# Performance work log

Measured on AMD Instinct MI355X. Metric: run time of the kernel, lower is better.

The kernel has to match this reference:

```python
import jax, jax.numpy as jnp
import numpy as np

MIN_NEAR = 0.05
DENSITY_SCALE = 1.0
BOUND = 1.0  # spherical scene bounds radius
GEO = 15


def _density_mlp(x, dW1, db1, dW2, db2, dW3, db3):
    h = jax.nn.relu(x @ dW1 + db1)
    h = jax.nn.relu(h @ dW2 + db2)
    h = h @ dW3 + db3  # [M, 1+GEO]
    sigma = jnp.exp(jnp.clip(h[..., 0], -15.0, 15.0))  # trunc_exp
    return sigma, h[..., 1:]


def _color_mlp(d, geo, cW1, cb1, cW2, cb2, cW3, cb3):
    h = jnp.concatenate([d, geo], axis=-1)
    h = jax.nn.relu(h @ cW1 + cb1)
    h = jax.nn.relu(h @ cW2 + cb2)
    return jax.nn.sigmoid(h @ cW3 + cb3)


def _comp_weights(deltas, sigmas):
    # alpha compositing: w_i = alpha_i * prod_{j<i}(1 - alpha_j)
    alphas = 1.0 - jnp.exp(-deltas * sigmas)
    trans = jnp.cumprod(
        jnp.concatenate([jnp.ones_like(alphas[:, :1]), 1.0 - alphas + 1e-15], axis=-1),
        axis=-1)[:, :-1]
    return alphas * trans


def _sample_pdf(bins, weights, n_samples):
    # deterministic importance resampling (eval mode); bins [N,T-1], weights [N,T-2]
    weights = weights + 1e-5
    pdf = weights / jnp.sum(weights, axis=-1, keepdims=True)
    cdf = jnp.cumsum(pdf, axis=-1)
    cdf = jnp.concatenate([jnp.zeros_like(cdf[:, :1]), cdf], axis=-1)  # [N, T-1]
    u = jnp.linspace(0.5 / n_samples, 1.0 - 0.5 / n_samples, n_samples)
    u = jnp.broadcast_to(u, (bins.shape[0], n_samples))
    inds = jax.vmap(lambda c, uu: jnp.searchsorted(c, uu, side='right'))(cdf, u)
    below = jnp.clip(inds - 1, 0, cdf.shape[-1] - 1)
    above = jnp.clip(inds, 0, cdf.shape[-1] - 1)
    cdf_g0 = jnp.take_along_axis(cdf, below, axis=-1)
    cdf_g1 = jnp.take_along_axis(cdf, above, axis=-1)
    bmax = bins.shape[-1] - 1
    bins_g0 = jnp.take_along_axis(bins, jnp.clip(below, 0, bmax), axis=-1)
    bins_g1 = jnp.take_along_axis(bins, jnp.clip(above, 0, bmax), axis=-1)
    denom = jnp.where(cdf_g1 - cdf_g0 < 1e-5, 1.0, cdf_g1 - cdf_g0)
    t = (u - cdf_g0) / denom
    return bins_g0 + t * (bins_g1 - bins_g0)


def _run(rays_o, rays_d, dW1, db1, dW2, db2, dW3, db3,
         cW1, cb1, cW2, cb2, cW3, cb3, num_steps, upsample_steps):
    N = rays_o.shape[0]
    # get_z_val_bounds: ray/sphere intersection, sphere radius BOUND at origin
    b = jnp.sum(rays_o * rays_d, axis=-1)
    c = jnp.sum(rays_o * rays_o, axis=-1) - BOUND ** 2
    disc = jnp.maximum(b * b - c, 0.0)
    z_max = jnp.maximum(-b + jnp.sqrt(disc), MIN_NEAR + 1e-3)
    z_min = jnp.full_like(z_max, MIN_NEAR)
    # get_foreground_z_vals: per-ray linspace (perturb=False)
    t = jnp.linspace(0.0, 1.0, num_steps)
    z_vals = z_min[:, None] + (z_max - z_min)[:, None] * t[None, :]
    z_vals = jnp.clip(z_vals, z_min[:, None], z_max[:, None])
    xyzs = rays_o[:, None, :] + rays_d[:, None, :] * z_vals[..., None]
    sigma, geo = _density_mlp(xyzs.reshape(-1, 3), dW1, db1, dW2, db2, dW3, db3)
    sigma = sigma.reshape(N, num_steps)
    geo = geo.reshape(N, num_steps, GEO)

    # upsample_z_values: importance resampling from coarse weights
    deltas = z_vals[:, 1:] - z_vals[:, :-1]
    aug = jnp.concatenate([deltas, deltas[:, -1:]], axis=-1)
    w_coarse = _comp_weights(aug, DENSITY_SCALE * sigma)
    z_mid = 0.5 * (z_vals[:, :-1] + z_vals[:, 1:])
    new_z = jax.lax.stop_gradient(_sample_pdf(z_mid, w_coarse[:, 1:-1], upsample_steps))
    new_xyzs = rays_o[:, None, :] + rays_d[:, None, :] * new_z[..., None]
    new_sigma, new_geo = _density_mlp(new_xyzs.reshape(-1, 3), dW1, db1, dW2, db2, dW3, db3)
    new_sigma = new_sigma.reshape(N, upsample_steps)
    new_geo = new_geo.reshape(N, upsample_steps, GEO)

    # sort/gather merge of coarse + fine samples
    z_all = jnp.concatenate([z_vals, new_z], axis=1)
    order = jnp.argsort(z_all, axis=1)
    z_vals = jnp.take_along_axis(z_all, order, axis=1)  # [N, T]
    xyzs = jnp.take_along_axis(jnp.concatenate([xyzs, new_xyzs], axis=1), order[..., None], axis=1)
    sigma = jnp.take_along_axis(jnp.concatenate([sigma, new_sigma], axis=1), order, axis=1)
    geo = jnp.take_along_axis(jnp.concatenate([geo, new_geo], axis=1), order[..., None], axis=1)

    deltas = z_vals[:, 1:] - z_vals[:, :-1]
    aug = jnp.concatenate([deltas, deltas[:, -1:]], axis=-1)
    weights = _comp_weights(aug, DENSITY_SCALE * sigma)  # [N, T]

    mask = weights > 1e-4
    dirs = jnp.broadcast_to(rays_d[:, None, :], xyzs.shape).reshape(-1, 3)
    rgb = _color_mlp(dirs, geo.reshape(-1, GEO), cW1, cb1, cW2, cb2, cW3, cb3)
    rgbs = jnp.where(mask.reshape(-1, 1), rgb, 0.0).reshape(N, -1, 3)

    weights_sum = jnp.sum(weights, axis=-1)
    depth = jnp.sum(weights * z_vals, axis=-1)
    image = jnp.sum(weights[..., None] * rgbs, axis=-2)
    bg = 206.0 / 255.0
    image = image + (1.0 - weights_sum)[..., None] * bg

    # pairwise distortion loss (the (z_shifted - z_shifted) term in the source is identically zero)
    sample_dist = 1.0 / num_steps
    z_shift = jnp.concatenate([z_vals[:, 1:], jnp.full((N, 1), sample_dist, z_vals.dtype)], axis=-1)
    mid_zs = 0.5 * z_vals + 0.5 * z_shift
    pair = jnp.abs(mid_zs[:, None, :] - mid_zs[:, :, None]) * (weights[:, None, :] * weights[:, :, None])
    loss = jnp.sum(pair, axis=(1, 2)) / (depth + 1e-6)
    loss = jnp.where(loss < 1e-3, 0.0, loss)  # cutoff
    return jnp.concatenate([image, depth[:, None], loss[:, None]], axis=-1)  # [N, 5]


def setup_inputs() -> dict:
    key = jax.random.key(0)
    ks = jax.random.split(key, 16)
    N, H = 2048, 256
    rays_o = 0.1 * jax.random.normal(ks[0], (N, 3), jnp.float32)  # near scene centre
    rd = jax.random.normal(ks[1], (N, 3), jnp.float32)
    rays_d = rd / jnp.linalg.norm(rd, axis=-1, keepdims=True)

    def w(k, shape):
        return jax.random.normal(k, shape, jnp.float32) * (1.0 / np.sqrt(shape[0]))

    return {
        'rays_o': rays_o, 'rays_d': rays_d,
        'dW1': w(ks[2], (3, H)), 'db1': jnp.zeros(H, jnp.float32),
        'dW2': w(ks[3], (H, H)), 'db2': jnp.zeros(H, jnp.float32),
        'dW3': w(ks[4], (H, 1 + GEO)), 'db3': jnp.zeros(1 + GEO, jnp.float32),
        'cW1': w(ks[5], (3 + GEO, H)), 'cb1': jnp.zeros(H, jnp.float32),
        'cW2': w(ks[6], (H, H)), 'cb2': jnp.zeros(H, jnp.float32),
        'cW3': w(ks[7], (H, 3)), 'cb3': jnp.zeros(3, jnp.float32),
        'num_steps': 128, 'upsample_steps': 128,
    }


def reference(rays_o, rays_d, dW1, db1, dW2, db2, dW3, db3,
              cW1, cb1, cW2, cb2, cW3, cb3, num_steps, upsample_steps):
    return _run(rays_o, rays_d, dW1, db1, dW2, db2, dW3, db3,
                cW1, cb1, cW2, cb2, cW3, cb3, num_steps, upsample_steps)
```

## Files before the change

kernel.cpp:

```cpp
#include <hip/hip_runtime.h>


typedef float f32x4 __attribute__((ext_vector_type(4)));
typedef __bf16 bf16x8 __attribute__((ext_vector_type(8)));
typedef __bf16 bf16x4 __attribute__((ext_vector_type(4)));
typedef unsigned short u16x8 __attribute__((ext_vector_type(8)));
typedef unsigned short u16x4 __attribute__((ext_vector_type(4)));

#define NRAYS 2048
#define NSTEP 128
#define MIN_NEAR 0.05f

#define OFF_D1 0
#define OFF_D2 8192
#define OFF_D3 73728
#define OFF_C1 77824
#define OFF_C2 86016
#define OFF_C3 151552
#define PACK_TOTAL 155648

__device__ __forceinline__ unsigned short f2bf(float f) {
  __bf16 h = (__bf16)f;
  return __builtin_bit_cast(unsigned short, h);
}
__device__ __forceinline__ u16x4 pack4(float a, float b, float c, float d) {
  bf16x4 h;
  h[0] = (__bf16)a; h[1] = (__bf16)b; h[2] = (__bf16)c; h[3] = (__bf16)d;
  return __builtin_bit_cast(u16x4, h);
}

__device__ __forceinline__ float ray_z(const float* __restrict__ ro,
                                       const float* __restrict__ rd, int r, int i) {
  float ox = ro[r * 3], oy = ro[r * 3 + 1], oz = ro[r * 3 + 2];
  float dx = rd[r * 3], dy = rd[r * 3 + 1], dz = rd[r * 3 + 2];
  float b = ox * dx + oy * dy + oz * dz;
  float c = ox * ox + oy * oy + oz * oz - 1.0f;
  float disc = fmaxf(b * b - c, 0.0f);
  float zmax = fmaxf(-b + sqrtf(disc), MIN_NEAR + 1e-3f);
  float zmin = MIN_NEAR;
  float tt = (float)i / 127.0f;
  float zz = zmin + (zmax - zmin) * tt;
  return fminf(fmaxf(zz, zmin), zmax);
}

__device__ __forceinline__ float wave_iscan(float v, int lane) {
#pragma unroll
  for (int off = 1; off < 64; off <<= 1) {
    float y = __shfl_up(v, off, 64);
    if (lane >= off) v += y;
  }
  return v;
}
__device__ __forceinline__ float block_iscan(float v, float* part, int lane, int wid) {
  float s = wave_iscan(v, lane);
  if (lane == 63) part[wid] = s;
  __syncthreads();
  float pre = 0.f;
  if (wid > 0) pre += part[0];
  if (wid > 1) pre += part[1];
  if (wid > 2) pre += part[2];
  return s + pre;
}

__device__ __forceinline__ void pack_std(const float* __restrict__ W,
                                         unsigned short* __restrict__ dst,
                                         int idx, int K, int Norig, int NT) {
  int per = NT * 512;
  int kt = idx / per, rm = idx % per;
  int nt = rm >> 9, lane = (rm >> 3) & 63, j = rm & 7;
  int k = kt * 32 + ((lane >> 4) << 3) + j;
  int n = nt * 16 + (lane & 15);
  float v = (k < K && n < Norig) ? W[k * Norig + n] : 0.0f;
  dst[idx] = f2bf(v);
}

__global__ void k_pack_all(const float* __restrict__ dW1, const float* __restrict__ dW2,
                           const float* __restrict__ dW3, const float* __restrict__ cW1,
                           const float* __restrict__ cW2, const float* __restrict__ cW3,
                           unsigned short* __restrict__ Wp) {
  int idx = blockIdx.x * 256 + threadIdx.x;
  if (idx < OFF_D2) {
    pack_std(dW1, Wp + OFF_D1, idx - OFF_D1, 3, 256, 16);
  } else if (idx < OFF_D3) {
    pack_std(dW2, Wp + OFF_D2, idx - OFF_D2, 256, 256, 16);
  } else if (idx < OFF_C1) {
    int j2 = idx - OFF_D3;
    int lane = (j2 >> 3) & 63, jj = j2 & 7, kt = j2 >> 9;
    int k = kt * 32 + ((lane >> 4) << 3) + jj;
    int n = lane & 15;
    Wp[idx] = f2bf(dW3[k * 16 + ((n + 1) & 15)]);
  } else if (idx < OFF_C2) {
    int j2 = idx - OFF_C1;
    int nt = j2 >> 9, lane = (j2 >> 3) & 63, jj = j2 & 7;
    int k = ((lane >> 4) << 3) + jj;
    int n = nt * 16 + (lane & 15);
    float v = 0.0f;
    if (k < 15) v = cW1[(3 + k) * 256 + n];
    else if (k >= 16 && k < 19) v = cW1[(k - 16) * 256 + n];
    Wp[idx] = f2bf(v);
  } else if (idx < OFF_C3) {
    pack_std(cW2, Wp + OFF_C2, idx - OFF_C2, 256, 256, 16);
  } else if (idx < PACK_TOTAL) {
    pack_std(cW3, Wp + OFF_C3, idx - OFF_C3, 256, 3, 1);
  }
}


__device__ __forceinline__ void mlp_l1(const unsigned short* xb, unsigned short* buf,
                                       const bf16x8 (&w1r)[4], const float* sb1,
                                       int wid, int quad, int col) {
#pragma unroll
  for (int h = 0; h < 2; ++h) {
    f32x4 acc[8];
#pragma unroll
    for (int i = 0; i < 8; ++i) acc[i] = (f32x4){0.f, 0.f, 0.f, 0.f};
    int p0 = (h * 2) * 16 + col, p1 = (h * 2 + 1) * 16 + col;
    bf16x8 x0 = *reinterpret_cast<const bf16x8*>(&xb[p0 * 32 + ((quad ^ (p0 & 3)) * 8)]);
    bf16x8 x1 = *reinterpret_cast<const bf16x8*>(&xb[p1 * 32 + ((quad ^ (p1 & 3)) * 8)]);
#pragma unroll
    for (int ntl = 0; ntl < 4; ++ntl) {
      acc[ntl * 2 + 0] = __builtin_amdgcn_mfma_f32_16x16x32_bf16(w1r[ntl], x0, acc[ntl * 2 + 0], 0, 0, 0);
      acc[ntl * 2 + 1] = __builtin_amdgcn_mfma_f32_16x16x32_bf16(w1r[ntl], x1, acc[ntl * 2 + 1], 0, 0, 0);
    }
#pragma unroll
    for (int ntl = 0; ntl < 4; ++ntl) {
      int n = (wid * 4 + ntl) * 16 + quad * 4;
      f32x4 bv = *reinterpret_cast<const f32x4*>(&sb1[n]);
#pragma unroll
      for (int j = 0; j < 2; ++j) {
        int p = (h * 2 + j) * 16 + col;
        *reinterpret_cast<u16x4*>(&buf[p * 256 + (((n >> 3) ^ (p & 31)) * 8) + (n & 7)]) =
            pack4(fmaxf(acc[ntl * 2 + j][0] + bv[0], 0.f), fmaxf(acc[ntl * 2 + j][1] + bv[1], 0.f),
                  fmaxf(acc[ntl * 2 + j][2] + bv[2], 0.f), fmaxf(acc[ntl * 2 + j][3] + bv[3], 0.f));
      }
    }
  }
}

__device__ __forceinline__ void l2_half_compute(const unsigned short* buf,
                                                const bf16x8 (&w2r)[8][4],
                                                f32x4 (&acc)[8], int h, int quad, int col) {
#pragma unroll
  for (int i = 0; i < 8; ++i) acc[i] = (f32x4){0.f, 0.f, 0.f, 0.f};
#pragma unroll
  for (int kt = 0; kt < 8; ++kt) {
    int p0 = (h * 2) * 16 + col, p1 = (h * 2 + 1) * 16 + col;
    bf16x8 x0 = *reinterpret_cast<const bf16x8*>(&buf[p0 * 256 + (((kt * 4 + quad) ^ (p0 & 31)) * 8)]);
    bf16x8 x1 = *reinterpret_cast<const bf16x8*>(&buf[p1 * 256 + (((kt * 4 + quad) ^ (p1 & 31)) * 8)]);
#pragma unroll
    for (int ntl = 0; ntl < 4; ++ntl) {
      acc[ntl * 2 + 0] = __builtin_amdgcn_mfma_f32_16x16x32_bf16(w2r[kt][ntl], x0, acc[ntl * 2 + 0], 0, 0, 0);
      acc[ntl * 2 + 1] = __builtin_amdgcn_mfma_f32_16x16x32_bf16(w2r[kt][ntl], x1, acc[ntl * 2 + 1], 0, 0, 0);
    }
  }
}

__device__ __forceinline__ void l2_half_write(unsigned short* buf, const f32x4 (&acc)[8],
                                              const float* sb2, int h, int wid, int quad, int col) {
#pragma unroll
  for (int ntl = 0; ntl < 4; ++ntl) {
    int n = (wid * 4 + ntl) * 16 + quad * 4;
    f32x4 bv = *reinterpret_cast<const f32x4*>(&sb2[n]);
#pragma unroll
    for (int j = 0; j < 2; ++j) {
      int p = (h * 2 + j) * 16 + col;
      *reinterpret_cast<u16x4*>(&buf[p * 256 + (((n >> 3) ^ (p & 31)) * 8) + (n & 7)]) =
          pack4(fmaxf(acc[ntl * 2 + j][0] + bv[0], 0.f), fmaxf(acc[ntl * 2 + j][1] + bv[1], 0.f),
                fmaxf(acc[ntl * 2 + j][2] + bv[2], 0.f), fmaxf(acc[ntl * 2 + j][3] + bv[3], 0.f));
    }
  }
}

template <bool FIRST>
__global__ __launch_bounds__(256, 2)
void k_density(const float* __restrict__ ro, const float* __restrict__ rd,
               const float* __restrict__ zin,
               const unsigned short* __restrict__ Wp1, const float* __restrict__ b1,
               const unsigned short* __restrict__ Wp2, const float* __restrict__ b2,
               const unsigned short* __restrict__ Wp3, const float* __restrict__ b3,
               unsigned short* __restrict__ gout, float* __restrict__ sig,
               float* __restrict__ z_f) {
  __shared__ __align__(16) unsigned short buf[64 * 256];
  __shared__ __align__(16) unsigned short xb[64 * 32];
  __shared__ __align__(16) unsigned short sW3[4096];
  __shared__ __align__(16) float sb1[256];
  __shared__ __align__(16) float sb2[256];
  __shared__ __align__(16) float sb3[16];
  __shared__ __align__(16) float ssig[256];
  __shared__ __align__(16) float sred[16];
  const int t = threadIdx.x;
  const int lane = t & 63, wid = t >> 6, quad = lane >> 4, col = lane & 15;
  const int p_ = t >> 2, g_ = t & 3;

  sb1[t] = b1[t];
  sb2[t] = b2[t];
  if (t < 16) sb3[t] = b3[(t + 1) & 15];
  { const u16x8* s = (const u16x8*)Wp3; u16x8* d = (u16x8*)sW3;
    d[t] = s[t]; d[t + 256] = s[t + 256]; }

  bf16x8 w1r[4], w2r[8][4];
#pragma unroll
  for (int ntl = 0; ntl < 4; ++ntl)
    w1r[ntl] = *reinterpret_cast<const bf16x8*>(Wp1 + ((wid * 4 + ntl) * 64 + lane) * 8);
#pragma unroll
  for (int kt = 0; kt < 8; ++kt)
#pragma unroll
    for (int ntl = 0; ntl < 4; ++ntl)
      w2r[kt][ntl] = *reinterpret_cast<const bf16x8*>(Wp2 + ((kt * 16 + wid * 4 + ntl) * 64 + lane) * 8);

#pragma unroll 1
  for (int tt = 0; tt < 4; ++tt) {
    const int P0 = blockIdx.x * 256 + tt * 64;
    {
      u16x8 pk = {0, 0, 0, 0, 0, 0, 0, 0};
      if (g_ == 0) {
        int P = P0 + p_;
        int rr_ = P >> 7, ii = P & 127;
        float zz;
        if constexpr (FIRST) zz = ray_z(ro, rd, rr_, ii);
        else zz = zin[P];
        pk[0] = f2bf(ro[rr_ * 3 + 0] + rd[rr_ * 3 + 0] * zz);
        pk[1] = f2bf(ro[rr_ * 3 + 1] + rd[rr_ * 3 + 1] * zz);
        pk[2] = f2bf(ro[rr_ * 3 + 2] + rd[rr_ * 3 + 2] * zz);
      }
      *reinterpret_cast<u16x8*>(&xb[p_ * 32 + ((g_ ^ (p_ & 3)) * 8)]) = pk;
    }
    __syncthreads();
    mlp_l1(xb, buf, w1r, sb1, wid, quad, col);
    __syncthreads();
    f32x4 acc[8];
    l2_half_compute(buf, w2r, acc, 0, quad, col);
    __syncthreads();
    l2_half_write(buf, acc, sb2, 0, wid, quad, col);
    l2_half_compute(buf, w2r, acc, 1, quad, col);
    __syncthreads();
    l2_half_write(buf, acc, sb2, 1, wid, quad, col);
    __syncthreads();
    {
      const int p = wid * 16 + col;
      f32x4 a3 = {0.f, 0.f, 0.f, 0.f};
#pragma unroll
      for (int kt = 0; kt < 8; ++kt) {
        bf16x8 w = *reinterpret_cast<const bf16x8*>(&sW3[(kt * 64 + lane) * 8]);
        bf16x8 xx = *reinterpret_cast<const bf16x8*>(&buf[p * 256 + (((kt * 4 + quad) ^ (p & 31)) * 8)]);
        a3 = __builtin_amdgcn_mfma_f32_16x16x32_bf16(w, xx, a3, 0, 0, 0);
      }
      int n0 = quad * 4;
      float v0 = a3[0] + sb3[n0], v1 = a3[1] + sb3[n0 + 1];
      float v2 = a3[2] + sb3[n0 + 2], v3 = a3[3] + sb3[n0 + 3];
      if (quad == 3) {
        float sgm = __expf(fminf(fmaxf(v3, -15.f), 15.f));
        sig[P0 + p] = sgm;
        if constexpr (FIRST) ssig[tt * 64 + p] = sgm;
        v3 = 0.0f;
      }
      *reinterpret_cast<u16x4*>(gout + (size_t)(P0 + p) * 16 + n0) = pack4(v0, v1, v2, v3);
    }
  }

  if constexpr (FIRST) {
    __syncthreads();
    float* psz = reinterpret_cast<float*>(buf);
    float* pmid = psz + 256;
    float* pcdf = psz + 512;
    float* psw = psz + 768;
    const int segw = t >> 7;
    const int i = t & 127;
    const int seg = segw * 128;
    const int rg = blockIdx.x * 2 + segw;
    float zi = ray_z(ro, rd, rg, i);
    psz[seg + i] = zi;
    float sgv = ssig[t];
    __syncthreads();
    float aug = (i < 127) ? psz[seg + i + 1] - zi : psz[seg + 127] - psz[seg + 126];
    float alpha = 1.0f - __expf(-aug * sgv);
    float lt = __logf(1.0f - alpha + 1e-15f);
    float s = wave_iscan(lt, lane);
    if (lane == 63) sred[wid] = s;
    __syncthreads();
    if (wid & 1) s += sred[wid - 1];
    float w = alpha * __expf(s - lt);
    psw[seg + i] = w;
    if (i < 127) pmid[seg + i] = 0.5f * (zi + psz[seg + i + 1]);
    __syncthreads();
    float v2s = (i < 126) ? psw[seg + i + 1] + 1e-5f : 0.f;
    float s2 = wave_iscan(v2s, lane);
    if (lane == 63) sred[8 + wid] = s2;
    __syncthreads();
    if (wid & 1) s2 += sred[8 + wid - 1];
    psw[seg + i] = s2;
    __syncthreads();
    float total = psw[seg + 125];
    if (i <= 126) pcdf[seg + i] = (i == 0) ? 0.f : psw[seg + i - 1] / total;
    __syncthreads();
    const float lo = 0.5f / 128.0f, hi = 1.0f - 0.5f / 128.0f;
    float u = lo + (hi - lo) * ((float)i / 127.0f);
    int loI = 0, hiI = 127;
    while (loI < hiI) {
      int mid = (loI + hiI) >> 1;
      if (pcdf[seg + mid] > u) hiI = mid; else loI = mid + 1;
    }
    int below = loI - 1; if (below < 0) below = 0; if (below > 126) below = 126;
    int above = loI;     if (above > 126) above = 126;
    float c0 = pcdf[seg + below], c1 = pcdf[seg + above];
    float b0v = pmid[seg + below], b1v = pmid[seg + above];
    float dn = c1 - c0; if (dn < 1e-5f) dn = 1.0f;
    float ttt = (u - c0) / dn;
    z_f[rg * NSTEP + i] = b0v + ttt * (b1v - b0v);
  }
}

__global__ __launch_bounds__(256, 2)
void k_mcf(const float* __restrict__ ro, const float* __restrict__ rd,
           const float* __restrict__ z_f,
           const float* __restrict__ sigc, const float* __restrict__ sigf,
           const unsigned short* __restrict__ goutc, const unsigned short* __restrict__ goutf,
           const unsigned short* __restrict__ Wp1, const float* __restrict__ cb1,
           const unsigned short* __restrict__ Wp2, const float* __restrict__ cb2,
           const unsigned short* __restrict__ Wp3, const float* __restrict__ cb3,
           float* __restrict__ out) {
  __shared__ __align__(16) unsigned short buf[64 * 256];
  __shared__ __align__(16) unsigned short xb[64 * 32];
  __shared__ __align__(16) unsigned short sW3[4096];
  __shared__ __align__(16) float sb1[256];
  __shared__ __align__(16) float sb2[256];
  __shared__ __align__(16) float szm[256];
  __shared__ __align__(16) float swgt[256];
  __shared__ __align__(16) float srgb[768];
  __shared__ __align__(16) float sred[48];
  __shared__ unsigned short sord[256];
  const int t = threadIdx.x;
  const int lane = t & 63, wid = t >> 6, quad = lane >> 4, col = lane & 15;
  const int p_ = t >> 2, g_ = t & 3;
  const int r = blockIdx.x;

  sb1[t] = cb1[t];
  sb2[t] = cb2[t];
  { const u16x8* s = (const u16x8*)Wp3; u16x8* d = (u16x8*)sW3;
    d[t] = s[t]; d[t + 256] = s[t + 256]; }

  bf16x8 w1r[4], w2r[8][4];
#pragma unroll
  for (int ntl = 0; ntl < 4; ++ntl)
    w1r[ntl] = *reinterpret_cast<const bf16x8*>(Wp1 + ((wid * 4 + ntl) * 64 + lane) * 8);
#pragma unroll
  for (int kt = 0; kt < 8; ++kt)
#pragma unroll
    for (int ntl = 0; ntl < 4; ++ntl)
      w2r[kt][ntl] = *reinterpret_cast<const bf16x8*>(Wp2 + ((kt * 16 + wid * 4 + ntl) * 64 + lane) * 8);

  float* szc = reinterpret_cast<float*>(buf);
  float* szf = szc + 128;
  if (t < 128) szc[t] = ray_z(ro, rd, r, t);
  else szf[t - 128] = z_f[r * NSTEP + (t - 128)];
  __syncthreads();
  int pos; float myz;
  if (t < 128) {
    myz = szc[t];
    int lo = 0, hi = 128;
    while (lo < hi) { int m = (lo + hi) >> 1; if (szf[m] < myz) lo = m + 1; else hi = m; }
    pos = t + lo;
  } else {
    int j = t - 128; myz = szf[j];
    int lo = 0, hi = 128;
    while (lo < hi) { int m = (lo + hi) >> 1; if (szc[m] <= myz) lo = m + 1; else hi = m; }
    pos = j + lo;
  }
  szm[pos] = myz; sord[pos] = (unsigned short)t;
  __syncthreads();
  int srci = sord[t];
  float sg = (srci < 128) ? sigc[r * NSTEP + srci] : sigf[r * NSTEP + (srci - 128)];
  float zt = szm[t];
  float aug = (t < 255) ? szm[t + 1] - zt : szm[255] - szm[254];
  float alpha = 1.0f - __expf(-aug * sg);
  float lt = __logf(1.0f - alpha + 1e-15f);
  float incl = block_iscan(lt, sred, lane, wid);
  swgt[t] = alpha * __expf(incl - lt);
  __syncthreads();

  float dv0 = rd[r * 3], dv1 = rd[r * 3 + 1], dv2 = rd[r * 3 + 2];
  u16x8 dirpk = {f2bf(dv0), f2bf(dv1), f2bf(dv2), 0, 0, 0, 0, 0};
  u16x8 gx = {0, 0, 0, 0, 0, 0, 0, 0};
  float wgtv = 0.0f;
  {
    if (g_ < 2) {
      int s0 = sord[p_];
      const unsigned short* gs = ((s0 < 128) ? goutc : goutf)
          + ((size_t)(r * NSTEP + (s0 & 127)) * 16) + g_ * 8;
      gx = *reinterpret_cast<const u16x8*>(gs);
    } else if (g_ == 2) {
      gx = dirpk;
    } else {
      wgtv = swgt[p_];
    }
  }
#pragma unroll 1
  for (int tt = 0; tt < 4; ++tt) {
    const int haveNext = (tt < 3);
    int go = __syncthreads_or((g_ == 3) && (wgtv > 1e-4f));
    int ordn = 0; float wgtn = 0.0f;
    u16x8 gxn = {0, 0, 0, 0, 0, 0, 0, 0};
    if (go) {
      *reinterpret_cast<u16x8*>(&xb[p_ * 32 + ((g_ ^ (p_ & 3)) * 8)]) = gx;
      __syncthreads();
      mlp_l1(xb, buf, w1r, sb1, wid, quad, col);
      __syncthreads();
    }
    if (haveNext) {
      int Pn = (tt + 1) * 64 + p_;
      if (g_ < 2) ordn = sord[Pn];
      else if (g_ == 2) gxn = dirpk;
      else wgtn = swgt[Pn];
    }
    f32x4 acc[8];
    if (go) {
      l2_half_compute(buf, w2r, acc, 0, quad, col);
      __syncthreads();
      l2_half_write(buf, acc, sb2, 0, wid, quad, col);
    }
    if (haveNext && g_ < 2) {
      const unsigned short* gs = ((ordn < 128) ? goutc : goutf)
          + ((size_t)(r * NSTEP + (ordn & 127)) * 16) + g_ * 8;
      gxn = *reinterpret_cast<const u16x8*>(gs);
    }
    if (go) {
      l2_half_compute(buf, w2r, acc, 1, quad, col);
      __syncthreads();
      l2_half_write(buf, acc, sb2, 1, wid, quad, col);
      __syncthreads();
      {
        const int p = wid * 16 + col;
        f32x4 a3 = {0.f, 0.f, 0.f, 0.f};
#pragma unroll
        for (int kt = 0; kt < 8; ++kt) {
          bf16x8 w = *reinterpret_cast<const bf16x8*>(&sW3[(kt * 64 + lane) * 8]);
          bf16x8 xx = *reinterpret_cast<const bf16x8*>(&buf[p * 256 + (((kt * 4 + quad) ^ (p & 31)) * 8)]);
          a3 = __builtin_amdgcn_mfma_f32_16x16x32_bf16(w, xx, a3, 0, 0, 0);
        }
        if (quad == 0) {
          int pi = tt * 64 + p;
          srgb[pi * 3 + 0] = 1.0f / (1.0f + __expf(-(a3[0] + cb3[0])));
          srgb[pi * 3 + 1] = 1.0f / (1.0f + __expf(-(a3[1] + cb3[1])));
          srgb[pi * 3 + 2] = 1.0f / (1.0f + __expf(-(a3[2] + cb3[2])));
        }
      }
    }
    gx = gxn; wgtv = wgtn;
  }

  __syncthreads();
  float ztf = szm[t], wtf = swgt[t];
  float znext = (t < 255) ? szm[t + 1] : (1.0f / 128.0f);
  float mt = 0.5f * ztf + 0.5f * znext;
  float cr = 0.f, cg = 0.f, cbl = 0.f;
  if (wtf > 1e-4f) { cr = srgb[t * 3]; cg = srgb[t * 3 + 1]; cbl = srgb[t * 3 + 2]; }
  if (t == 255) { sred[36] = mt; sred[37] = wtf; }
  float wm = (t < 255) ? wtf : 0.f;
  float Pw = block_iscan(wm, sred, lane, wid);
  float Ps = block_iscan(wm * mt, sred + 4, lane, wid);
  float W254 = sred[0] + sred[1] + sred[2] + sred[3];
  float S254 = sred[4] + sred[5] + sred[6] + sred[7];
  float m255 = sred[36], w255 = sred[37];
  float contrib = 0.f;
  if (t < 255)
    contrib = wtf * (mt * (2.f * Pw - W254) - (2.f * Ps - S254))
            + 2.f * wtf * fabsf(mt - m255) * w255;
  float vals[6] = {wtf, wtf * ztf, wtf * cr, wtf * cg, wtf * cbl, contrib};
#pragma unroll
  for (int k = 0; k < 6; ++k) {
    float v = vals[k];
#pragma unroll
    for (int m = 1; m < 64; m <<= 1) v += __shfl_xor(v, m, 64);
    if (lane == 0) sred[8 + k * 4 + wid] = v;
  }
  __syncthreads();
  if (t == 0) {
    float a6[6];
#pragma unroll
    for (int k = 0; k < 6; ++k)
      a6[k] = sred[8 + k * 4] + sred[8 + k * 4 + 1] + sred[8 + k * 4 + 2] + sred[8 + k * 4 + 3];
    const float bgc = 206.0f / 255.0f;
    float wsum = a6[0], depth = a6[1];
    float loss = a6[5] / (depth + 1e-6f);
    if (loss < 1e-3f) loss = 0.0f;
    out[r * 5 + 0] = a6[2] + (1.0f - wsum) * bgc;
    out[r * 5 + 1] = a6[3] + (1.0f - wsum) * bgc;
    out[r * 5 + 2] = a6[4] + (1.0f - wsum) * bgc;
    out[r * 5 + 3] = depth;
    out[r * 5 + 4] = loss;
  }
}

extern "C" void kernel_launch(void* const* d_in, const int* in_sizes, int n_in,
                              void* d_out, int out_size, void* d_ws, size_t ws_size,
                              hipStream_t stream) {
  const float* rays_o = (const float*)d_in[0];
  const float* rays_d = (const float*)d_in[1];
  const float* dW1 = (const float*)d_in[2];
  const float* db1 = (const float*)d_in[3];
  const float* dW2 = (const float*)d_in[4];
  const float* db2 = (const float*)d_in[5];
  const float* dW3 = (const float*)d_in[6];
  const float* db3 = (const float*)d_in[7];
  const float* cW1 = (const float*)d_in[8];
  const float* cb1 = (const float*)d_in[9];
  const float* cW2 = (const float*)d_in[10];
  const float* cb2 = (const float*)d_in[11];
  const float* cW3 = (const float*)d_in[12];
  const float* cb3 = (const float*)d_in[13];

  char* ws = (char*)d_ws;
  size_t off = 0;
  auto alloc = [&](size_t bytes) -> void* {
    void* p = ws + off;
    off += (bytes + 255) & ~(size_t)255;
    return p;
  };
  unsigned short* Wp = (unsigned short*)alloc((size_t)PACK_TOTAL * 2);
  unsigned short* goutc = (unsigned short*)alloc((size_t)NRAYS * NSTEP * 16 * 2);
  unsigned short* goutf = (unsigned short*)alloc((size_t)NRAYS * NSTEP * 16 * 2);
  float* sigc = (float*)alloc((size_t)NRAYS * NSTEP * 4);
  float* sigf = (float*)alloc((size_t)NRAYS * NSTEP * 4);
  float* z_f  = (float*)alloc((size_t)NRAYS * NSTEP * 4);
  (void)ws_size; (void)in_sizes; (void)n_in; (void)out_size;

  k_pack_all<<<PACK_TOTAL / 256, 256, 0, stream>>>(dW1, dW2, dW3, cW1, cW2, cW3, Wp);

  k_density<true><<<(NRAYS * NSTEP) / 256, 256, 0, stream>>>(
      rays_o, rays_d, nullptr,
      Wp + OFF_D1, db1, Wp + OFF_D2, db2, Wp + OFF_D3, db3, goutc, sigc, z_f);
  k_density<false><<<(NRAYS * NSTEP) / 256, 256, 0, stream>>>(
      rays_o, rays_d, z_f,
      Wp + OFF_D1, db1, Wp + OFF_D2, db2, Wp + OFF_D3, db3, goutf, sigf, nullptr);
  k_mcf<<<NRAYS, 256, 0, stream>>>(
      rays_o, rays_d, z_f, sigc, sigf, goutc, goutf,
      Wp + OFF_C1, cb1, Wp + OFF_C2, cb2, Wp + OFF_C3, cb3, (float*)d_out);
}
```

Measured before the change: 272.2 us.

## Split MLP N-tiles across 8 waves with 512-thread blocks

```diff
diff --git a/kernel.cpp b/kernel.cpp
--- a/kernel.cpp
+++ b/kernel.cpp
@@ -51,14 +51,14 @@
   }
   return v;
 }
-__device__ __forceinline__ float block_iscan(float v, float* part, int lane, int wid) {
+__device__ __forceinline__ float block_iscan8(float v, float* part, int lane, int wid) {
   float s = wave_iscan(v, lane);
   if (lane == 63) part[wid] = s;
   __syncthreads();
   float pre = 0.f;
-  if (wid > 0) pre += part[0];
-  if (wid > 1) pre += part[1];
-  if (wid > 2) pre += part[2];
+#pragma unroll
+  for (int w = 0; w < 7; ++w)
+    if (w < wid) pre += part[w];
   return s + pre;
 }
 
@@ -107,24 +107,24 @@
 
 
 __device__ __forceinline__ void mlp_l1(const unsigned short* xb, unsigned short* buf,
-                                       const bf16x8 (&w1r)[4], const float* sb1,
+                                       const bf16x8 (&w1r)[2], const float* sb1,
                                        int wid, int quad, int col) {
 #pragma unroll
   for (int h = 0; h < 2; ++h) {
-    f32x4 acc[8];
-#pragma unroll
-    for (int i = 0; i < 8; ++i) acc[i] = (f32x4){0.f, 0.f, 0.f, 0.f};
+    f32x4 acc[4];
+#pragma unroll
+    for (int i = 0; i < 4; ++i) acc[i] = (f32x4){0.f, 0.f, 0.f, 0.f};
     int p0 = (h * 2) * 16 + col, p1 = (h * 2 + 1) * 16 + col;
     bf16x8 x0 = *reinterpret_cast<const bf16x8*>(&xb[p0 * 32 + ((quad ^ (p0 & 3)) * 8)]);
     bf16x8 x1 = *reinterpret_cast<const bf16x8*>(&xb[p1 * 32 + ((quad ^ (p1 & 3)) * 8)]);
 #pragma unroll
-    for (int ntl = 0; ntl < 4; ++ntl) {
+    for (int ntl = 0; ntl < 2; ++ntl) {
       acc[ntl * 2 + 0] = __builtin_amdgcn_mfma_f32_16x16x32_bf16(w1r[ntl], x0, acc[ntl * 2 + 0], 0, 0, 0);
       acc[ntl * 2 + 1] = __builtin_amdgcn_mfma_f32_16x16x32_bf16(w1r[ntl], x1, acc[ntl * 2 + 1], 0, 0, 0);
     }
 #pragma unroll
-    for (int ntl = 0; ntl < 4; ++ntl) {
-      int n = (wid * 4 + ntl) * 16 + quad * 4;
+    for (int ntl = 0; ntl < 2; ++ntl) {
+      int n = (wid * 2 + ntl) * 16 + quad * 4;
       f32x4 bv = *reinterpret_cast<const f32x4*>(&sb1[n]);
 #pragma unroll
       for (int j = 0; j < 2; ++j) {
@@ -138,28 +138,28 @@
 }
 
 __device__ __forceinline__ void l2_half_compute(const unsigned short* buf,
-                                                const bf16x8 (&w2r)[8][4],
-                                                f32x4 (&acc)[8], int h, int quad, int col) {
-#pragma unroll
-  for (int i = 0; i < 8; ++i) acc[i] = (f32x4){0.f, 0.f, 0.f, 0.f};
+                                                const bf16x8 (&w2r)[8][2],
+                                                f32x4 (&acc)[4], int h, int quad, int col) {
+#pragma unroll
+  for (int i = 0; i < 4; ++i) acc[i] = (f32x4){0.f, 0.f, 0.f, 0.f};
 #pragma unroll
   for (int kt = 0; kt < 8; ++kt) {
     int p0 = (h * 2) * 16 + col, p1 = (h * 2 + 1) * 16 + col;
     bf16x8 x0 = *reinterpret_cast<const bf16x8*>(&buf[p0 * 256 + (((kt * 4 + quad) ^ (p0 & 31)) * 8)]);
     bf16x8 x1 = *reinterpret_cast<const bf16x8*>(&buf[p1 * 256 + (((kt * 4 + quad) ^ (p1 & 31)) * 8)]);
 #pragma unroll
-    for (int ntl = 0; ntl < 4; ++ntl) {
+    for (int ntl = 0; ntl < 2; ++ntl) {
       acc[ntl * 2 + 0] = __builtin_amdgcn_mfma_f32_16x16x32_bf16(w2r[kt][ntl], x0, acc[ntl * 2 + 0], 0, 0, 0);
       acc[ntl * 2 + 1] = __builtin_amdgcn_mfma_f32_16x16x32_bf16(w2r[kt][ntl], x1, acc[ntl * 2 + 1], 0, 0, 0);
     }
   }
 }
 
-__device__ __forceinline__ void l2_half_write(unsigned short* buf, const f32x4 (&acc)[8],
+__device__ __forceinline__ void l2_half_write(unsigned short* buf, const f32x4 (&acc)[4],
                                               const float* sb2, int h, int wid, int quad, int col) {
 #pragma unroll
-  for (int ntl = 0; ntl < 4; ++ntl) {
-    int n = (wid * 4 + ntl) * 16 + quad * 4;
+  for (int ntl = 0; ntl < 2; ++ntl) {
+    int n = (wid * 2 + ntl) * 16 + quad * 4;
     f32x4 bv = *reinterpret_cast<const f32x4*>(&sb2[n]);
 #pragma unroll
     for (int j = 0; j < 2; ++j) {
@@ -172,7 +172,7 @@
 }
 
 template <bool FIRST>
-__global__ __launch_bounds__(256, 2)
+__global__ __launch_bounds__(512, 4)
 void k_density(const float* __restrict__ ro, const float* __restrict__ rd,
                const float* __restrict__ zin,
                const unsigned short* __restrict__ Wp1, const float* __restrict__ b1,
@@ -192,26 +192,28 @@
   const int lane = t & 63, wid = t >> 6, quad = lane >> 4, col = lane & 15;
   const int p_ = t >> 2, g_ = t & 3;
 
-  sb1[t] = b1[t];
-  sb2[t] = b2[t];
-  if (t < 16) sb3[t] = b3[(t + 1) & 15];
-  { const u16x8* s = (const u16x8*)Wp3; u16x8* d = (u16x8*)sW3;
-    d[t] = s[t]; d[t + 256] = s[t + 256]; }
-
-  bf16x8 w1r[4], w2r[8][4];
-#pragma unroll
-  for (int ntl = 0; ntl < 4; ++ntl)
-    w1r[ntl] = *reinterpret_cast<const bf16x8*>(Wp1 + ((wid * 4 + ntl) * 64 + lane) * 8);
+  if (t < 256) {
+    sb1[t] = b1[t];
+    sb2[t] = b2[t];
+    if (t < 16) sb3[t] = b3[(t + 1) & 15];
+    const u16x8* s = (const u16x8*)Wp3; u16x8* d = (u16x8*)sW3;
+    d[t] = s[t]; d[t + 256] = s[t + 256];
+  }
+
+  bf16x8 w1r[2], w2r[8][2];
+#pragma unroll
+  for (int ntl = 0; ntl < 2; ++ntl)
+    w1r[ntl] = *reinterpret_cast<const bf16x8*>(Wp1 + ((wid * 2 + ntl) * 64 + lane) * 8);
 #pragma unroll
   for (int kt = 0; kt < 8; ++kt)
 #pragma unroll
-    for (int ntl = 0; ntl < 4; ++ntl)
-      w2r[kt][ntl] = *reinterpret_cast<const bf16x8*>(Wp2 + ((kt * 16 + wid * 4 + ntl) * 64 + lane) * 8);
+    for (int ntl = 0; ntl < 2; ++ntl)
+      w2r[kt][ntl] = *reinterpret_cast<const bf16x8*>(Wp2 + ((kt * 16 + wid * 2 + ntl) * 64 + lane) * 8);
 
 #pragma unroll 1
   for (int tt = 0; tt < 4; ++tt) {
     const int P0 = blockIdx.x * 256 + tt * 64;
-    {
+    if (t < 256) {
       u16x8 pk = {0, 0, 0, 0, 0, 0, 0, 0};
       if (g_ == 0) {
         int P = P0 + p_;
@@ -228,7 +230,7 @@
     __syncthreads();
     mlp_l1(xb, buf, w1r, sb1, wid, quad, col);
     __syncthreads();
-    f32x4 acc[8];
+    f32x4 acc[4];
     l2_half_compute(buf, w2r, acc, 0, quad, col);
     __syncthreads();
     l2_half_write(buf, acc, sb2, 0, wid, quad, col);
@@ -236,7 +238,7 @@
     __syncthreads();
     l2_half_write(buf, acc, sb2, 1, wid, quad, col);
     __syncthreads();
-    {
+    if (wid < 4) {
       const int p = wid * 16 + col;
       f32x4 a3 = {0.f, 0.f, 0.f, 0.f};
 #pragma unroll
@@ -264,53 +266,67 @@
     float* pmid = psz + 256;
     float* pcdf = psz + 512;
     float* psw = psz + 768;
-    const int segw = t >> 7;
+    const int segw = (t >> 7) & 1;
     const int i = t & 127;
     const int seg = segw * 128;
     const int rg = blockIdx.x * 2 + segw;
-    float zi = ray_z(ro, rd, rg, i);
-    psz[seg + i] = zi;
-    float sgv = ssig[t];
-    __syncthreads();
-    float aug = (i < 127) ? psz[seg + i + 1] - zi : psz[seg + 127] - psz[seg + 126];
-    float alpha = 1.0f - __expf(-aug * sgv);
-    float lt = __logf(1.0f - alpha + 1e-15f);
+    const bool act = (t < 256);
+    float zi = 0.f, sgv = 0.f;
+    if (act) {
+      zi = ray_z(ro, rd, rg, i);
+      psz[seg + i] = zi;
+      sgv = ssig[t];
+    }
+    __syncthreads();
+    float lt = 0.f, alpha = 0.f;
+    if (act) {
+      float aug = (i < 127) ? psz[seg + i + 1] - zi : psz[seg + 127] - psz[seg + 126];
+      alpha = 1.0f - __expf(-aug * sgv);
+      lt = __logf(1.0f - alpha + 1e-15f);
+    }
     float s = wave_iscan(lt, lane);
     if (lane == 63) sred[wid] = s;
     __syncthreads();
     if (wid & 1) s += sred[wid - 1];
-    float w = alpha * __expf(s - lt);
-    psw[seg + i] = w;
-    if (i < 127) pmid[seg + i] = 0.5f * (zi + psz[seg + i + 1]);
-    __syncthreads();
-    float v2s = (i < 126) ? psw[seg + i + 1] + 1e-5f : 0.f;
+    if (act) {
+      float w = alpha * __expf(s - lt);
+      psw[seg + i] = w;
+      if (i < 127) pmid[seg + i] = 0.5f * (zi + psz[seg + i + 1]);
+    }
+    __syncthreads();
+    float v2s = (act && i < 126) ? psw[seg + i + 1] + 1e-5f : 0.f;
     float s2 = wave_iscan(v2s, lane);
     if (lane == 63) sred[8 + wid] = s2;
     __syncthreads();
     if (wid & 1) s2 += sred[8 + wid - 1];
-    psw[seg + i] = s2;
-    __syncthreads();
-    float total = psw[seg + 125];
-    if (i <= 126) pcdf[seg + i] = (i == 0) ? 0.f : psw[seg + i - 1] / total;
-    __syncthreads();
-    const float lo = 0.5f / 128.0f, hi = 1.0f - 0.5f / 128.0f;
-    float u = lo + (hi - lo) * ((float)i / 127.0f);
-    int loI = 0, hiI = 127;
-    while (loI < hiI) {
-      int mid = (loI + hiI) >> 1;
-      if (pcdf[seg + mid] > u) hiI = mid; else loI = mid + 1;
-    }
-    int below = loI - 1; if (below < 0) below = 0; if (below > 126) below = 126;
-    int above = loI;     if (above > 126) above = 126;
-    float c0 = pcdf[seg + below], c1 = pcdf[seg + above];
-    float b0v = pmid[seg + below], b1v = pmid[seg + above];
-    float dn = c1 - c0; if (dn < 1e-5f) dn = 1.0f;
-    float ttt = (u - c0) / dn;
-    z_f[rg * NSTEP + i] = b0v + ttt * (b1v - b0v);
-  }
-}
-
-__global__ __launch_bounds__(256, 2)
+    if (act) psw[seg + i] = s2;
+    __syncthreads();
+    if (act) {
+      float total = psw[seg + 125];
+      if (i <= 126) pcdf[seg + i] = (i == 0) ? 0.f : psw[seg + i - 1] / total;
+      if (i < 127) ;
+    }
+    __syncthreads();
+    if (act) {
+      const float lo = 0.5f / 128.0f, hi = 1.0f - 0.5f / 128.0f;
+      float u = lo + (hi - lo) * ((float)i / 127.0f);
+      int loI = 0, hiI = 127;
+      while (loI < hiI) {
+        int mid = (loI + hiI) >> 1;
+        if (pcdf[seg + mid] > u) hiI = mid; else loI = mid + 1;
+      }
+      int below = loI - 1; if (below < 0) below = 0; if (below > 126) below = 126;
+      int above = loI;     if (above > 126) above = 126;
+      float c0 = pcdf[seg + below], c1 = pcdf[seg + above];
+      float b0v = pmid[seg + below], b1v = pmid[seg + above];
+      float dn = c1 - c0; if (dn < 1e-5f) dn = 1.0f;
+      float ttt = (u - c0) / dn;
+      z_f[rg * NSTEP + i] = b0v + ttt * (b1v - b0v);
+    }
+  }
+}
+
+__global__ __launch_bounds__(512, 4)
 void k_mcf(const float* __restrict__ ro, const float* __restrict__ rd,
            const float* __restrict__ z_f,
            const float* __restrict__ sigc, const float* __restrict__ sigf,
@@ -334,101 +350,88 @@
   const int p_ = t >> 2, g_ = t & 3;
   const int r = blockIdx.x;
 
-  sb1[t] = cb1[t];
-  sb2[t] = cb2[t];
-  { const u16x8* s = (const u16x8*)Wp3; u16x8* d = (u16x8*)sW3;
-    d[t] = s[t]; d[t + 256] = s[t + 256]; }
-
-  bf16x8 w1r[4], w2r[8][4];
-#pragma unroll
-  for (int ntl = 0; ntl < 4; ++ntl)
-    w1r[ntl] = *reinterpret_cast<const bf16x8*>(Wp1 + ((wid * 4 + ntl) * 64 + lane) * 8);
+  if (t < 256) {
+    sb1[t] = cb1[t];
+    sb2[t] = cb2[t];
+    const u16x8* s = (const u16x8*)Wp3; u16x8* d = (u16x8*)sW3;
+    d[t] = s[t]; d[t + 256] = s[t + 256];
+  }
+
+  bf16x8 w1r[2], w2r[8][2];
+#pragma unroll
+  for (int ntl = 0; ntl < 2; ++ntl)
+    w1r[ntl] = *reinterpret_cast<const bf16x8*>(Wp1 + ((wid * 2 + ntl) * 64 + lane) * 8);
 #pragma unroll
   for (int kt = 0; kt < 8; ++kt)
 #pragma unroll
-    for (int ntl = 0; ntl < 4; ++ntl)
-      w2r[kt][ntl] = *reinterpret_cast<const bf16x8*>(Wp2 + ((kt * 16 + wid * 4 + ntl) * 64 + lane) * 8);
+    for (int ntl = 0; ntl < 2; ++ntl)
+      w2r[kt][ntl] = *reinterpret_cast<const bf16x8*>(Wp2 + ((kt * 16 + wid * 2 + ntl) * 64 + lane) * 8);
 
   float* szc = reinterpret_cast<float*>(buf);
   float* szf = szc + 128;
   if (t < 128) szc[t] = ray_z(ro, rd, r, t);
-  else szf[t - 128] = z_f[r * NSTEP + (t - 128)];
+  else if (t < 256) szf[t - 128] = z_f[r * NSTEP + (t - 128)];
   __syncthreads();
-  int pos; float myz;
-  if (t < 128) {
-    myz = szc[t];
-    int lo = 0, hi = 128;
-    while (lo < hi) { int m = (lo + hi) >> 1; if (szf[m] < myz) lo = m + 1; else hi = m; }
-    pos = t + lo;
-  } else {
-    int j = t - 128; myz = szf[j];
-    int lo = 0, hi = 128;
-    while (lo < hi) { int m = (lo + hi) >> 1; if (szc[m] <= myz) lo = m + 1; else hi = m; }
-    pos = j + lo;
-  }
-  szm[pos] = myz; sord[pos] = (unsigned short)t;
+  if (t < 256) {
+    int pos; float myz;
+    if (t < 128) {
+      myz = szc[t];
+      int lo = 0, hi = 128;
+      while (lo < hi) { int m = (lo + hi) >> 1; if (szf[m] < myz) lo = m + 1; else hi = m; }
+      pos = t + lo;
+    } else {
+      int j = t - 128; myz = szf[j];
+      int lo = 0, hi = 128;
+      while (lo < hi) { int m = (lo + hi) >> 1; if (szc[m] <= myz) lo = m + 1; else hi = m; }
+      pos = j + lo;
+    }
+    szm[pos] = myz; sord[pos] = (unsigned short)t;
+  }
   __syncthreads();
-  int srci = sord[t];
-  float sg = (srci < 128) ? sigc[r * NSTEP + srci] : sigf[r * NSTEP + (srci - 128)];
-  float zt = szm[t];
-  float aug = (t < 255) ? szm[t + 1] - zt : szm[255] - szm[254];
-  float alpha = 1.0f - __expf(-aug * sg);
-  float lt = __logf(1.0f - alpha + 1e-15f);
-  float incl = block_iscan(lt, sred, lane, wid);
-  swgt[t] = alpha * __expf(incl - lt);
+  float lt = 0.f, alpha = 0.f;
+  if (t < 256) {
+    int srci = sord[t];
+    float sg = (srci < 128) ? sigc[r * NSTEP + srci] : sigf[r * NSTEP + (srci - 128)];
+    float zt = szm[t];
+    float aug = (t < 255) ? szm[t + 1] - zt : szm[255] - szm[254];
+    alpha = 1.0f - __expf(-aug * sg);
+    lt = __logf(1.0f - alpha + 1e-15f);
+  }
+  float incl = block_iscan8(lt, sred, lane, wid);
+  if (t < 256) swgt[t] = alpha * __expf(incl - lt);
   __syncthreads();
 
   float dv0 = rd[r * 3], dv1 = rd[r * 3 + 1], dv2 = rd[r * 3 + 2];
   u16x8 dirpk = {f2bf(dv0), f2bf(dv1), f2bf(dv2), 0, 0, 0, 0, 0};
-  u16x8 gx = {0, 0, 0, 0, 0, 0, 0, 0};
-  float wgtv = 0.0f;
-  {
-    if (g_ < 2) {
-      int s0 = sord[p_];
-      const unsigned short* gs = ((s0 < 128) ? goutc : goutf)
-          + ((size_t)(r * NSTEP + (s0 & 127)) * 16) + g_ * 8;
-      gx = *reinterpret_cast<const u16x8*>(gs);
-    } else if (g_ == 2) {
-      gx = dirpk;
-    } else {
-      wgtv = swgt[p_];
-    }
-  }
 #pragma unroll 1
   for (int tt = 0; tt < 4; ++tt) {
-    const int haveNext = (tt < 3);
-    int go = __syncthreads_or((g_ == 3) && (wgtv > 1e-4f));
-    int ordn = 0; float wgtn = 0.0f;
-    u16x8 gxn = {0, 0, 0, 0, 0, 0, 0, 0};
+    int pred = (t < 64) && (swgt[tt * 64 + t] > 1e-4f);
+    int go = __syncthreads_or(pred);
     if (go) {
-      *reinterpret_cast<u16x8*>(&xb[p_ * 32 + ((g_ ^ (p_ & 3)) * 8)]) = gx;
+      if (t < 256) {
+        u16x8 pk = {0, 0, 0, 0, 0, 0, 0, 0};
+        if (g_ < 2) {
+          int s0 = sord[tt * 64 + p_];
+          const unsigned short* gs = ((s0 < 128) ? goutc : goutf)
+              + ((size_t)(r * NSTEP + (s0 & 127)) * 16) + g_ * 8;
+          pk = *reinterpret_cast<const u16x8*>(gs);
+        } else if (g_ == 2) {
+          pk = dirpk;
+        }
+        *reinterpret_cast<u16x8*>(&xb[p_ * 32 + ((g_ ^ (p_ & 3)) * 8)]) = pk;
+      }
       __syncthreads();
       mlp_l1(xb, buf, w1r, sb1, wid, quad, col);
       __syncthreads();
-    }
-    if (haveNext) {
-      int Pn = (tt + 1) * 64 + p_;
-      if (g_ < 2) ordn = sord[Pn];
-      else if (g_ == 2) gxn = dirpk;
-      else wgtn = swgt[Pn];
-    }
-    f32x4 acc[8];
-    if (go) {
+      f32x4 acc[4];
       l2_half_compute(buf, w2r, acc, 0, quad, col);
       __syncthreads();
       l2_half_write(buf, acc, sb2, 0, wid, quad, col);
-    }
-    if (haveNext && g_ < 2) {
-      const unsigned short* gs = ((ordn < 128) ? goutc : goutf)
-          + ((size_t)(r * NSTEP + (ordn & 127)) * 16) + g_ * 8;
-      gxn = *reinterpret_cast<const u16x8*>(gs);
-    }
-    if (go) {
       l2_half_compute(buf, w2r, acc, 1, quad, col);
       __syncthreads();
       l2_half_write(buf, acc, sb2, 1, wid, quad, col);
       __syncthreads();
-      {
+      if (wid < 4) {
         const int p = wid * 16 + col;
         f32x4 a3 = {0.f, 0.f, 0.f, 0.f};
 #pragma unroll
@@ -445,22 +448,25 @@
         }
       }
     }
-    gx = gxn; wgtv = wgtn;
   }
 
   __syncthreads();
-  float ztf = szm[t], wtf = swgt[t];
-  float znext = (t < 255) ? szm[t + 1] : (1.0f / 128.0f);
-  float mt = 0.5f * ztf + 0.5f * znext;
+  float ztf = 0.f, wtf = 0.f, mt = 0.f;
   float cr = 0.f, cg = 0.f, cbl = 0.f;
-  if (wtf > 1e-4f) { cr = srgb[t * 3]; cg = srgb[t * 3 + 1]; cbl = srgb[t * 3 + 2]; }
-  if (t == 255) { sred[36] = mt; sred[37] = wtf; }
+  if (t < 256) {
+    ztf = szm[t]; wtf = swgt[t];
+    float znext = (t < 255) ? szm[t + 1] : (1.0f / 128.0f);
+    mt = 0.5f * ztf + 0.5f * znext;
+    if (wtf > 1e-4f) { cr = srgb[t * 3]; cg = srgb[t * 3 + 1]; cbl = srgb[t * 3 + 2]; }
+    if (t == 255) { sred[40] = mt; sred[41] = wtf; }
+  }
   float wm = (t < 255) ? wtf : 0.f;
-  float Pw = block_iscan(wm, sred, lane, wid);
-  float Ps = block_iscan(wm * mt, sred + 4, lane, wid);
-  float W254 = sred[0] + sred[1] + sred[2] + sred[3];
-  float S254 = sred[4] + sred[5] + sred[6] + sred[7];
-  float m255 = sred[36], w255 = sred[37];
+  float Pw = block_iscan8(wm, sred, lane, wid);
+  float Ps = block_iscan8(wm * mt, sred + 8, lane, wid);
+  float W254 = 0.f, S254 = 0.f;
+#pragma unroll
+  for (int w = 0; w < 4; ++w) { W254 += sred[w]; S254 += sred[8 + w]; }
+  float m255 = sred[40], w255 = sred[41];
   float contrib = 0.f;
   if (t < 255)
     contrib = wtf * (mt * (2.f * Pw - W254) - (2.f * Ps - S254))
@@ -471,14 +477,14 @@
     float v = vals[k];
 #pragma unroll
     for (int m = 1; m < 64; m <<= 1) v += __shfl_xor(v, m, 64);
-    if (lane == 0) sred[8 + k * 4 + wid] = v;
+    if (lane == 0 && wid < 4) sred[16 + k * 4 + wid] = v;
   }
   __syncthreads();
   if (t == 0) {
     float a6[6];
 #pragma unroll
     for (int k = 0; k < 6; ++k)
-      a6[k] = sred[8 + k * 4] + sred[8 + k * 4 + 1] + sred[8 + k * 4 + 2] + sred[8 + k * 4 + 3];
+      a6[k] = sred[16 + k * 4] + sred[16 + k * 4 + 1] + sred[16 + k * 4 + 2] + sred[16 + k * 4 + 3];
     const float bgc = 206.0f / 255.0f;
     float wsum = a6[0], depth = a6[1];
     float loss = a6[5] / (depth + 1e-6f);
@@ -526,13 +532,13 @@
 
   k_pack_all<<<PACK_TOTAL / 256, 256, 0, stream>>>(dW1, dW2, dW3, cW1, cW2, cW3, Wp);
 
-  k_density<true><<<(NRAYS * NSTEP) / 256, 256, 0, stream>>>(
+  k_density<true><<<(NRAYS * NSTEP) / 256, 512, 0, stream>>>(
       rays_o, rays_d, nullptr,
       Wp + OFF_D1, db1, Wp + OFF_D2, db2, Wp + OFF_D3, db3, goutc, sigc, z_f);
-  k_density<false><<<(NRAYS * NSTEP) / 256, 256, 0, stream>>>(
+  k_density<false><<<(NRAYS * NSTEP) / 256, 512, 0, stream>>>(
       rays_o, rays_d, z_f,
       Wp + OFF_D1, db1, Wp + OFF_D2, db2, Wp + OFF_D3, db3, goutf, sigf, nullptr);
-  k_mcf<<<NRAYS, 256, 0, stream>>>(
+  k_mcf<<<NRAYS, 512, 0, stream>>>(
       rays_o, rays_d, z_f, sigc, sigf, goutc, goutf,
       Wp + OFF_C1, cb1, Wp + OFF_C2, cb2, Wp + OFF_C3, cb3, (float*)d_out);
 }
```

Measured after the change: 328.9 us. +20.8%, slower.
